# Kernel tuning notes

Measured on AMD Instinct MI355X. Metric: run time of the kernel, lower is better.

The kernel has to match this reference:

```python
import jax, jax.numpy as jnp
import numpy as np

SEQ, SUB, B, V = 32, 16, 512, 258
U = SEQ // SUB
Z, CH, CO, DH = 512, 1024, 512, 1024


def _lstm_cell(x, h, c, Wi, Wh, bi, bh):
    # torch gate order: input, forget, cell, output
    g = x @ Wi + h @ Wh + bi + bh  # [B, 4H]
    i, f, gg, o = jnp.split(g, 4, axis=-1)
    c = jax.nn.sigmoid(f) * c + jax.nn.sigmoid(i) * jnp.tanh(gg)
    h = jax.nn.sigmoid(o) * jnp.tanh(c)
    return h, c


def _lstm2(xs, h1_0, p1, p2):
    # xs: [T,B,in]; h1_0: [B,H] layer-1 initial hidden.
    # Layer-2 hidden and both cell states start at zero (initialize_state in torch code).
    z0 = jnp.zeros_like(h1_0)
    def step(carry, x):
        h1, c1, h2, c2 = carry
        h1, c1 = _lstm_cell(x, h1, c1, *p1)
        h2, c2 = _lstm_cell(h1, h2, c2, *p2)
        return (h1, c1, h2, c2), h2
    _, hs = jax.lax.scan(step, (h1_0, z0, z0, z0), xs)
    return hs  # [T,B,H] top-layer hidden states


def setup_inputs() -> dict:
    key = jax.random.key(0)
    ks = iter(jax.random.split(key, 40))
    def w(shape, s=0.05):
        return jax.random.normal(next(ks), shape, dtype=jnp.float32) * s
    return {
        "z": jax.random.normal(next(ks), (B, Z), dtype=jnp.float32),
        "x": jax.random.uniform(next(ks), (SEQ, B, V), dtype=jnp.float32),
        "conductor_input": w((1, B, V)),
        "ci_W": w((Z, CH)), "ci_b": w((CH,)),
        "cW1i": w((V, 4 * CH)), "cW1h": w((CH, 4 * CH)), "cb1i": w((4 * CH,)), "cb1h": w((4 * CH,)),
        "cW2i": w((CH, 4 * CH)), "cW2h": w((CH, 4 * CH)), "cb2i": w((4 * CH,)), "cb2h": w((4 * CH,)),
        "co_W": w((CH, CO)), "co_b": w((CO,)),
        "di_W": w((CO, DH)), "di_b": w((DH,)),
        "dW1i": w((CO + V, 4 * DH)), "dW1h": w((DH, 4 * DH)), "db1i": w((4 * DH,)), "db1h": w((4 * DH,)),
        "dW2i": w((DH, 4 * DH)), "dW2h": w((DH, 4 * DH)), "db2i": w((4 * DH,)), "db2h": w((4 * DH,)),
        "fc_W": w((DH, V)), "fc_b": w((V,)),
    }


def reference(z, x, conductor_input, ci_W, ci_b, cW1i, cW1h, cb1i, cb1h, cW2i, cW2h, cb2i, cb2h, co_W, co_b, di_W, di_b, dW1i, dW1h, db1i, db1h, dW2i, dW2h, db2i, db2h, fc_W, fc_b):
    # --- conductor: 2-layer LSTM over U steps of a learned constant input ---
    h1 = jnp.tanh(z @ ci_W + ci_b)  # [B,CH] layer-1 init hidden
    cin = jnp.broadcast_to(conductor_input, (U, B, V))
    ch = _lstm2(cin, h1, (cW1i, cW1h, cb1i, cb1h), (cW2i, cW2h, cb2i, cb2h))  # [U,B,CH]
    c = ch @ co_W + co_b  # [U,B,CO]
    # --- decoder (teacher forcing): state resets each sub-sequence, so the U
    # segments of length SUB are independent given c -> vmap over segments ---
    sos = jnp.zeros((1, B, V), jnp.float32).at[:, :, 0].set(1.0)
    prev = jnp.concatenate([sos, x[:-1]], axis=0).reshape(U, SUB, B, V)
    cb = jnp.broadcast_to(c[:, None], (U, SUB, B, CO))
    dec_in = jnp.concatenate([cb, prev], axis=-1)  # [U,SUB,B,CO+V]
    def run_seg(xs, cj):
        h1_0 = jnp.tanh(cj @ di_W + di_b)  # [B,DH]
        return _lstm2(xs, h1_0, (dW1i, dW1h, db1i, db1h), (dW2i, dW2h, db2i, db2h))
    hs = jax.vmap(run_seg)(dec_in, c)  # [U,SUB,B,DH]
    logp = jax.nn.log_softmax(hs @ fc_W + fc_b, axis=-1)  # log(softmax(.)) fused
    return logp.reshape(SEQ, B, V).transpose(1, 0, 2)  # [B,SEQ,V]
```

## Files before the change

### kernel.cpp

```cpp
#include <hip/hip_runtime.h>
#include <cstddef>
#include <cstdint>


namespace {

typedef short s8v __attribute__((ext_vector_type(8)));
typedef float f4v __attribute__((ext_vector_type(4)));
typedef unsigned short ushort_t;

__device__ inline unsigned short f2bf(float f) {
    union { float f; unsigned u; } v; v.f = f;
    unsigned r = v.u + 0x7fff + ((v.u >> 16) & 1);
    return (unsigned short)(r >> 16);
}
__device__ inline float bf2f(ushort_t u) {
    union { unsigned u; float f; } v; v.u = ((unsigned)u) << 16; return v.f;
}
__device__ inline float sigm_f(float x) { return 1.f / (1.f + __expf(-x)); }
__device__ inline float tanh_f(float x) {
    const float e = __expf(2.f * fabsf(x));
    return copysignf(1.f - 2.f / (e + 1.f), x);
}

#define GLOAD_LDS(gp, lp)                                              \
    __builtin_amdgcn_global_load_lds(                                  \
        (const __attribute__((address_space(1))) void*)(gp),           \
        (__attribute__((address_space(3))) void*)(lp), 16, 0, 0)

__device__ __forceinline__ void gemm_core(
    const ushort_t* __restrict__ A1a, const ushort_t* __restrict__ A1b,
    int lda1, int K1, const ushort_t* __restrict__ W1,
    const ushort_t* __restrict__ A2, int lda2, int K2,
    const ushort_t* __restrict__ W2,
    int bm, int bn, ushort_t* lds, f4v acc[4][4])
{
    const int tid = threadIdx.x;
    const int wid = tid >> 6;
    const int lane = tid & 63;
    const int wr = wid >> 1, wc = wid & 1;
    const int lrow = lane & 15, lkg = lane >> 4;

    const int n1 = K1 >> 5;
    const int n2 = (W2 != nullptr) ? (K2 >> 5) : 0;
    const int nt = n1 + n2;

    const int row0 = wid * 16 + (lane >> 2);
    const int row1 = row0 + 64;
    const int src0 = (((lane & 3) ^ ((row0 >> 1) & 3)) << 3);
    const int src1 = (((lane & 3) ^ ((row1 >> 1) & 3)) << 3);

    auto arow = [&](const ushort_t* Aa, const ushort_t* Ab, int lda,
                    int r) -> const ushort_t* {
        return (Ab != nullptr && r >= 512) ? Ab + (size_t)(r - 512) * lda
                                           : Aa + (size_t)r * lda;
    };
    const ushort_t* pA1q0 = arow(A1a, A1b, lda1, bm + row0) + src0;
    const ushort_t* pA1q1 = arow(A1a, A1b, lda1, bm + row1) + src1;
    const ushort_t* pA2q0 = nullptr;
    const ushort_t* pA2q1 = nullptr;
    if (n2 > 0) {
        pA2q0 = A2 + (size_t)(bm + row0) * lda2 + src0;
        pA2q1 = A2 + (size_t)(bm + row1) * lda2 + src1;
    }

    int sbuf = 2;
    auto stageA = [&](int idx, int buf) {
        const ushort_t *p0, *p1;
        if (idx < n1) { p0 = pA1q0 + (idx << 5); p1 = pA1q1 + (idx << 5); }
        else { const int i2 = idx - n1; p0 = pA2q0 + (i2 << 5); p1 = pA2q1 + (i2 << 5); }
        GLOAD_LDS(p0, lds + buf * 4096 + wid * 512);
        GLOAD_LDS(p1, lds + buf * 4096 + 2048 + wid * 512);
    };

    const int nb0 = (bn >> 4) + wc * 4;
    const ushort_t* W1l = W1 + (size_t)nb0 * n1 * 512 + lane * 8;
    const ushort_t* W2l = (n2 > 0) ? (W2 + (size_t)nb0 * n2 * 512 + lane * 8) : nullptr;

    auto loadB = [&](int t, s8v (&b)[4]) {
        const ushort_t* base; int kb, KB;
        if (t < n1) { base = W1l; kb = t; KB = n1; }
        else        { base = W2l; kb = t - n1; KB = n2; }
#pragma unroll
        for (int n = 0; n < 4; ++n)
            b[n] = *(const s8v*)(base + ((size_t)(n * KB + kb) << 9));
    };

    int aoff[4];
#pragma unroll
    for (int m = 0; m < 4; ++m) {
        const int r = wr * 64 + m * 16 + lrow;
        aoff[m] = r * 32 + ((lkg ^ ((r >> 1) & 3)) << 3);
    }

    s8v bA[4], bB[4];
    loadB(0, bA);
    stageA(0, 0);
    if (nt > 1) stageA(1, 1);

    int cbuf = 0;
    auto iter = [&](int t, s8v (&bcur)[4], s8v (&bnxt)[4]) {
        if (t + 1 < nt) loadB(t + 1, bnxt);
        if (t + 1 < nt) asm volatile("s_waitcnt vmcnt(6)" ::: "memory");
        else            asm volatile("s_waitcnt vmcnt(0)" ::: "memory");
        __builtin_amdgcn_s_barrier();
        __builtin_amdgcn_sched_barrier(0);
        if (t + 2 < nt) {
            stageA(t + 2, sbuf);
            sbuf = (sbuf == 2) ? 0 : sbuf + 1;
        }
        const ushort_t* L = lds + cbuf * 4096;
        s8v a[4];
#pragma unroll
        for (int m = 0; m < 4; ++m) a[m] = *(const s8v*)(L + aoff[m]);
        __builtin_amdgcn_s_setprio(1);
#pragma unroll
        for (int m = 0; m < 4; ++m)
#pragma unroll
            for (int n = 0; n < 4; ++n)
                acc[m][n] = __builtin_amdgcn_mfma_f32_16x16x32_bf16(
                    a[m], bcur[n], acc[m][n], 0, 0, 0);
        __builtin_amdgcn_s_setprio(0);
        cbuf = (cbuf == 2) ? 0 : cbuf + 1;
    };

    int t = 0;
    while (true) {
        iter(t, bA, bB); if (++t == nt) break;
        iter(t, bB, bA); if (++t == nt) break;
    }
}

template <int ACT>
__global__ __launch_bounds__(256, 2) void plain_gemm(
    const ushort_t* __restrict__ A, int lda, int K,
    const ushort_t* __restrict__ W,
    const float* __restrict__ bias, int bias_n,
    float* __restrict__ C, ushort_t* __restrict__ Cbf, int N)
{
    __shared__ __align__(16) ushort_t lds[3 * 4096];
    const int bm = blockIdx.x * 128, bn = blockIdx.y * 128;
    f4v acc[4][4] = {};
    gemm_core(A, nullptr, lda, K, W, nullptr, 0, 0, nullptr, bm, bn, lds, acc);

    const int tid = threadIdx.x, wid = tid >> 6, lane = tid & 63;
    const int wr = wid >> 1, wc = wid & 1, lrow = lane & 15, lkg = lane >> 4;
#pragma unroll
    for (int m = 0; m < 4; ++m) {
        const int row0 = bm + wr * 64 + m * 16 + lkg * 4;
#pragma unroll
        for (int n = 0; n < 4; ++n) {
            const int col = bn + wc * 64 + n * 16 + lrow;
            const float bv = (bias != nullptr && col < bias_n) ? bias[col] : 0.f;
#pragma unroll
            for (int r = 0; r < 4; ++r) {
                float v = acc[m][n][r] + bv;
                if (ACT == 1) v = tanh_f(v);
                const size_t o = (size_t)(row0 + r) * N + col;
                if (C != nullptr) C[o] = v;
                if (Cbf != nullptr) Cbf[o] = f2bf(v);
            }
        }
    }
}

struct Prob {
    const ushort_t* A1a; const ushort_t* A1b; int lda1; int K1;
    const ushort_t* B1t;
    const ushort_t* A2; int lda2; int K2; const ushort_t* B2t;
    const ushort_t* Dbf;
    const float* bias;
    float* cst;
    ushort_t* hout;
    ushort_t* hs;
    int step_s;
};

__global__ __launch_bounds__(256, 2) void lstm_step(Prob PA, int nxa, Prob PB,
                                                    int mshift)
{
    __shared__ __align__(16) ushort_t lds[3 * 4096];
    const int nblk = gridDim.x;
    const int wg = blockIdx.x;
    const int swz = (wg & 7) * (nblk >> 3) + (wg >> 3);
    const int nmb = 1 << mshift;
    const int nb = swz >> mshift;
    const int mb = swz & (nmb - 1);

    const bool isA = mb < nxa;
    const Prob& P = isA ? PA : PB;
    const int bm = (isA ? mb : mb - nxa) * 128;
    const int bn = nb * 128;

    f4v acc[4][4] = {};
    gemm_core(P.A1a, P.A1b, P.lda1, P.K1, P.B1t,
              P.A2, P.lda2, P.K2, P.B2t, bm, bn, lds, acc);

    const int tid = threadIdx.x, wid = tid >> 6, lane = tid & 63;
    const int wr = wid >> 1, wc = wid & 1, lrow = lane & 15, lkg = lane >> 4;
    const int colbase = bn + wc * 64;
    const int jb = (colbase >> 6) * 16 + lrow;

#pragma unroll
    for (int m = 0; m < 4; ++m) {
        const int row0 = bm + wr * 64 + m * 16 + lkg * 4;
#pragma unroll
        for (int r = 0; r < 4; ++r) {
            const int row = row0 + r;
            float g0 = acc[m][0][r], g1 = acc[m][1][r];
            float g2 = acc[m][2][r], g3 = acc[m][3][r];
            if (P.Dbf != nullptr) {
                const ushort_t* d = P.Dbf + (size_t)row * 4096 + colbase + lrow;
                g0 += bf2f(d[0]); g1 += bf2f(d[16]);
                g2 += bf2f(d[32]); g3 += bf2f(d[48]);
            }
            if (P.bias != nullptr) {
                const float* b = P.bias + colbase + lrow;
                g0 += b[0]; g1 += b[16]; g2 += b[32]; g3 += b[48];
            }
            const size_t ci = (size_t)row * 1024 + jb;
            const float cn = fmaf(sigm_f(g1), P.cst[ci], sigm_f(g0) * tanh_f(g2));
            const float hn = sigm_f(g3) * tanh_f(cn);
            P.cst[ci] = cn;
            const ushort_t hb = f2bf(hn);
            P.hout[ci] = hb;
            if (P.hs != nullptr) {
                size_t d;
                if (P.step_s >= 0) {
                    const int u = row >> 9, b = row & 511;
                    d = ((size_t)((u * 16 + P.step_s) * 512 + b) << 10) + jb;
                } else {
                    d = ci;
                }
                P.hs[d] = hb;
            }
        }
    }
}

template <int PERM>
__global__ __launch_bounds__(256) void pack_frag_bf16(
    const float* __restrict__ in, ushort_t* __restrict__ out,
    int K, int N, int Kp, int Np)
{
    __shared__ float tile[32][33];
    const int kb = blockIdx.x;
    const int np0 = blockIdx.y * 32;
    const int k0 = kb * 32;
    const int tx = threadIdx.x & 31;
    const int ty = threadIdx.x >> 5;
#pragma unroll
    for (int q = 0; q < 4; ++q) {
        const int k = k0 + ty + 8 * q;
        const int np = np0 + tx;
        int n;
        if (PERM) n = ((np >> 4) & 3) * 1024 + (np >> 6) * 16 + (np & 15);
        else      n = np;
        tile[ty + 8 * q][tx] = (k < K && n < N) ? in[(size_t)k * N + n] : 0.f;
    }
    __syncthreads();
    const int t = threadIdx.x;
    const int rec = t >> 7;
    const int lane = (t >> 1) & 63;
    const int half = t & 1;
    const size_t grec = (size_t)(np0 / 16 + rec) * (Kp / 32) + kb;
    const int kl = (lane >> 4) * 8 + half * 4;
    const int nl = rec * 16 + (lane & 15);
    ushort4 v;
    v.x = f2bf(tile[kl + 0][nl]);
    v.y = f2bf(tile[kl + 1][nl]);
    v.z = f2bf(tile[kl + 2][nl]);
    v.w = f2bf(tile[kl + 3][nl]);
    *(ushort4*)(out + (grec * 64 + lane) * 8 + half * 4) = v;
}

__global__ void convert_pad_bf16(const float* __restrict__ in,
                                 ushort_t* __restrict__ out,
                                 int K, int Kp, int total)
{
    const int idx = blockIdx.x * 256 + threadIdx.x;
    if (idx >= total) return;
    const int r = idx / Kp, k = idx - r * Kp;
    out[idx] = (k < K) ? f2bf(in[(size_t)r * K + k]) : (ushort_t)0;
}

__global__ void sos_init_bf16(ushort_t* __restrict__ sos)
{
    const int i = blockIdx.x * 256 + threadIdx.x;
    if (i < 512 * 320) sos[i] = ((i % 320) == 0) ? (ushort_t)0x3F80 : (ushort_t)0;
}

__global__ void permute_bias(const float* __restrict__ b1,
                             const float* __restrict__ b2,
                             float* __restrict__ out)
{
    const int c = blockIdx.x * 256 + threadIdx.x;
    if (c >= 4096) return;
    const int g = (c >> 4) & 3;
    const int j = (c >> 6) * 16 + (c & 15);
    out[c] = b1[g * 1024 + j] + b2[g * 1024 + j];
}

__global__ __launch_bounds__(256) void logsoftmax_kernel(
    const float* __restrict__ logits, float* __restrict__ out)
{
    const int row = blockIdx.x;
    const int tid = threadIdx.x;
    const float* L = logits + (size_t)row * 384;
    const int t = row >> 9;
    const int b = row & 511;
    float* O = out + ((size_t)b * 32 + t) * 258;

    const float x0 = L[tid];
    const float x1 = (tid < 2) ? L[256 + tid] : -1e30f;

    __shared__ float sm[4];
    float m = fmaxf(x0, x1);
#pragma unroll
    for (int off = 32; off > 0; off >>= 1) m = fmaxf(m, __shfl_down(m, off));
    if ((tid & 63) == 0) sm[tid >> 6] = m;
    __syncthreads();
    m = fmaxf(fmaxf(sm[0], sm[1]), fmaxf(sm[2], sm[3]));
    __syncthreads();

    float s = expf(x0 - m) + ((tid < 2) ? expf(x1 - m) : 0.f);
#pragma unroll
    for (int off = 32; off > 0; off >>= 1) s += __shfl_down(s, off);
    if ((tid & 63) == 0) sm[tid >> 6] = s;
    __syncthreads();
    s = sm[0] + sm[1] + sm[2] + sm[3];

    const float lse = m + logf(s);
    O[tid] = x0 - lse;
    if (tid < 2) O[256 + tid] = x1 - lse;
}

}

extern "C" void kernel_launch(void* const* d_in, const int* in_sizes, int n_in,
                              void* d_out, int out_size, void* d_ws, size_t ws_size,
                              hipStream_t stream)
{
    (void)in_sizes; (void)n_in; (void)out_size; (void)ws_size;

    const float* z    = (const float*)d_in[0];
    const float* x    = (const float*)d_in[1];
    const float* cin  = (const float*)d_in[2];
    const float* ciW  = (const float*)d_in[3];
    const float* cib  = (const float*)d_in[4];
    const float* cW1i = (const float*)d_in[5];
    const float* cW1h = (const float*)d_in[6];
    const float* cb1i = (const float*)d_in[7];
    const float* cb1h = (const float*)d_in[8];
    const float* cW2i = (const float*)d_in[9];
    const float* cW2h = (const float*)d_in[10];
    const float* cb2i = (const float*)d_in[11];
    const float* cb2h = (const float*)d_in[12];
    const float* coW  = (const float*)d_in[13];
    const float* cob  = (const float*)d_in[14];
    const float* diW  = (const float*)d_in[15];
    const float* dib  = (const float*)d_in[16];
    const float* dW1i = (const float*)d_in[17];
    const float* dW1h = (const float*)d_in[18];
    const float* db1i = (const float*)d_in[19];
    const float* db1h = (const float*)d_in[20];
    const float* dW2i = (const float*)d_in[21];
    const float* dW2h = (const float*)d_in[22];
    const float* db2i = (const float*)d_in[23];
    const float* db2h = (const float*)d_in[24];
    const float* fcW  = (const float*)d_in[25];
    const float* fcb  = (const float*)d_in[26];
    float* out = (float*)d_out;

    char* wsp = (char*)d_ws;
    size_t off = 0;
    auto allocf = [&](size_t n) { float* p = (float*)(wsp + off); off += n * 4; return p; };
    auto allocb = [&](size_t n) { ushort_t* p = (ushort_t*)(wsp + off); off += n * 2; return p; };

    float* cst = allocf((size_t)3 * 1024 * 1024 + 64);
    float* c1c = cst;
    float* c2c = cst + (size_t)512 * 1024;
    float* c1d = cst + (size_t)1024 * 1024;
    float* c2d = cst + (size_t)2 * 1024 * 1024;
    float* pb1c = allocf(4096);
    float* pb2c = allocf(4096);
    float* pb1d = allocf(4096);
    float* pb2d = allocf(4096);
    float* logits = allocf((size_t)16384 * 384);

    ushort_t* h2z  = allocb((size_t)2 * (512 + 1024) * 1024);
    ushort_t* hc2A = h2z;
    ushort_t* hc2B = h2z + (size_t)512 * 1024;
    ushort_t* h2dA = h2z + (size_t)2 * 512 * 1024;
    ushort_t* h2dB = h2z + (size_t)(2 * 512 + 1024) * 1024;

    ushort_t* hc1A = allocb((size_t)512 * 1024);
    ushort_t* hc1B = allocb((size_t)512 * 1024);
    ushort_t* h1dA = allocb((size_t)1024 * 1024);
    ushort_t* h1dB = allocb((size_t)1024 * 1024);

    ushort_t* zbf    = allocb((size_t)512 * 512);
    ushort_t* cinbf  = allocb((size_t)512 * 320);
    ushort_t* sosbf  = allocb((size_t)512 * 320);
    ushort_t* xbf    = allocb((size_t)16384 * 320);
    ushort_t* chbf   = allocb((size_t)1024 * 1024);
    ushort_t* ccode  = allocb((size_t)1024 * 512);
    ushort_t* cpre   = allocb((size_t)1024 * 4096);
    ushort_t* xW1c   = allocb((size_t)512 * 4096);
    ushort_t* hsbf   = allocb((size_t)16384 * 1024);

    ushort_t* ciWp  = allocb((size_t)1024 * 512);
    ushort_t* cW1ip = allocb((size_t)4096 * 320);
    ushort_t* cW1hp = allocb((size_t)4096 * 1024);
    ushort_t* cW2ip = allocb((size_t)4096 * 1024);
    ushort_t* cW2hp = allocb((size_t)4096 * 1024);
    ushort_t* coWp  = allocb((size_t)512 * 1024);
    ushort_t* dtopp = allocb((size_t)4096 * 512);
    ushort_t* dbotp = allocb((size_t)4096 * 320);
    ushort_t* diWp  = allocb((size_t)1024 * 512);
    ushort_t* dW1hp = allocb((size_t)4096 * 1024);
    ushort_t* dW2ip = allocb((size_t)4096 * 1024);
    ushort_t* dW2hp = allocb((size_t)4096 * 1024);
    ushort_t* fcWp  = allocb((size_t)384 * 1024);

    hipMemsetAsync(cst, 0, (size_t)3 * 1024 * 1024 * 4, stream);
    hipMemsetAsync(h2z, 0, (size_t)2 * (512 + 1024) * 1024 * 2, stream);

    auto pack = [&](const float* in, ushort_t* o, int K, int N, int Kp, int Np, int perm) {
        dim3 g(Kp / 32, Np / 32);
        if (perm) pack_frag_bf16<1><<<g, 256, 0, stream>>>(in, o, K, N, Kp, Np);
        else      pack_frag_bf16<0><<<g, 256, 0, stream>>>(in, o, K, N, Kp, Np);
    };
    pack(ciW, ciWp, 512, 1024, 512, 1024, 0);
    pack(cW1i, cW1ip, 258, 4096, 320, 4096, 1);
    pack(cW1h, cW1hp, 1024, 4096, 1024, 4096, 1);
    pack(cW2i, cW2ip, 1024, 4096, 1024, 4096, 1);
    pack(cW2h, cW2hp, 1024, 4096, 1024, 4096, 1);
    pack(coW, coWp, 1024, 512, 1024, 512, 0);
    pack(dW1i, dtopp, 512, 4096, 512, 4096, 1);
    pack(dW1i + (size_t)512 * 4096, dbotp, 258, 4096, 320, 4096, 1);
    pack(diW, diWp, 512, 1024, 512, 1024, 0);
    pack(dW1h, dW1hp, 1024, 4096, 1024, 4096, 1);
    pack(dW2i, dW2ip, 1024, 4096, 1024, 4096, 1);
    pack(dW2h, dW2hp, 1024, 4096, 1024, 4096, 1);
    pack(fcW, fcWp, 1024, 258, 1024, 384, 0);

    auto convert = [&](const float* in, ushort_t* o, int K, int Kp, int R) {
        const int total = R * Kp;
        convert_pad_bf16<<<dim3((total + 255) / 256), 256, 0, stream>>>(in, o, K, Kp, total);
    };
    convert(z, zbf, 512, 512, 512);
    convert(cin, cinbf, 258, 320, 512);
    convert(x, xbf, 258, 320, 16384);
    sos_init_bf16<<<dim3((512 * 320 + 255) / 256), 256, 0, stream>>>(sosbf);
    permute_bias<<<16, 256, 0, stream>>>(cb1i, cb1h, pb1c);
    permute_bias<<<16, 256, 0, stream>>>(cb2i, cb2h, pb2c);
    permute_bias<<<16, 256, 0, stream>>>(db1i, db1h, pb1d);
    permute_bias<<<16, 256, 0, stream>>>(db2i, db2h, pb2d);

    auto gemm = [&](int act, const ushort_t* A, int lda, int K, const ushort_t* W,
                    const float* bias, int bias_n,
                    float* C, ushort_t* Cbf, int M, int N) {
        dim3 g(M / 128, N / 128);
        if (act) plain_gemm<1><<<g, 256, 0, stream>>>(A, lda, K, W, bias, bias_n, C, Cbf, N);
        else     plain_gemm<0><<<g, 256, 0, stream>>>(A, lda, K, W, bias, bias_n, C, Cbf, N);
    };

    gemm(1, zbf, 512, 512, ciWp, cib, 1024, nullptr, hc1A, 512, 1024);
    gemm(0, cinbf, 320, 320, cW1ip, pb1c, 4096, nullptr, xW1c, 512, 4096);

    ushort_t* HC1[2] = {hc1A, hc1B};
    ushort_t* HC2[2] = {hc2A, hc2B};
    for (int k = 0; k <= 2; ++k) {
        Prob pa{}, pb{};
        int nxa = 0, nxb = 0;
        if (k < 2) {
            pa = {HC1[k & 1], nullptr, 1024, 1024, cW1hp,
                  nullptr, 0, 0, nullptr,
                  xW1c, nullptr, c1c, HC1[(k + 1) & 1], nullptr, -1};
            nxa = 4;
        }
        if (k >= 1) {
            pb = {HC1[k & 1], nullptr, 1024, 1024, cW2ip,
                  HC2[k & 1], 1024, 1024, cW2hp,
                  nullptr, pb2c, c2c, HC2[(k + 1) & 1],
                  chbf + (size_t)(k - 1) * 512 * 1024, -1};
            nxb = 4;
        }
        const int nmb = nxa + nxb;
        const int mshift = (nmb == 4) ? 2 : 3;
        lstm_step<<<dim3(nmb * 32), 256, 0, stream>>>(pa, nxa, pb, mshift);
    }

    gemm(0, chbf, 1024, 1024, coWp, cob, 512, nullptr, ccode, 1024, 512);
    gemm(0, ccode, 512, 512, dtopp, pb1d, 4096, nullptr, cpre, 1024, 4096);
    gemm(1, ccode, 512, 512, diWp, dib, 1024, nullptr, h1dA, 1024, 1024);

    ushort_t* H1[2] = {h1dA, h1dB};
    ushort_t* H2[2] = {h2dA, h2dB};
    for (int k = 0; k <= 16; ++k) {
        Prob pa{}, pb{};
        int nxa = 0, nxb = 0;
        if (k < 16) {
            const ushort_t* plo = (k == 0) ? sosbf : (xbf + (size_t)(k - 1) * 512 * 320);
            const ushort_t* phi = xbf + (size_t)(15 + k) * 512 * 320;
            pa = {plo, phi, 320, 320, dbotp,
                  H1[k & 1], 1024, 1024, dW1hp,
                  cpre, nullptr, c1d, H1[(k + 1) & 1], nullptr, -1};
            nxa = 8;
        }
        if (k >= 1) {
            pb = {H1[k & 1], nullptr, 1024, 1024, dW2ip,
                  H2[k & 1], 1024, 1024, dW2hp,
                  nullptr, pb2d, c2d, H2[(k + 1) & 1], hsbf, k - 1};
            nxb = 8;
        }
        const int nmb = nxa + nxb;
        const int mshift = (nmb == 8) ? 3 : 4;
        lstm_step<<<dim3(nmb * 32), 256, 0, stream>>>(pa, nxa, pb, mshift);
    }

    gemm(0, hsbf, 1024, 1024, fcWp, fcb, 258, logits, nullptr, 16384, 384);
    logsoftmax_kernel<<<dim3(16384), 256, 0, stream>>>(logits, out);
}
```

Measured before the change: 1.193 ms.

## Halve GEMM M-tile to 64 rows and deepen B-fragment prefetch to three stages

Shrinks the block tile from 128x128 to 64x128 in both the plain GEMM and the fused LSTM step kernel, doubling the number of workgroups per launch and raising launch bounds to allow 4 blocks per CU. The aim is better occupancy and more parallelism for the small per-step recurrent GEMMs, which previously launched too few blocks to fill the GPU. The B-operand register prefetch is also extended from double to triple buffering, issued two iterations ahead, with adjusted waitcnt thresholds. The trade-off is that each weight tile is loaded by twice as many blocks, lowering B reuse and increasing global/L2 traffic.

```diff
diff --git a/kernel.cpp b/kernel.cpp
--- a/kernel.cpp
+++ b/kernel.cpp
@@ -33,7 +33,7 @@
     int lda1, int K1, const ushort_t* __restrict__ W1,
     const ushort_t* __restrict__ A2, int lda2, int K2,
     const ushort_t* __restrict__ W2,
-    int bm, int bn, ushort_t* lds, f4v acc[4][4])
+    int bm, int bn, ushort_t* lds, f4v acc[2][4])
 {
     const int tid = threadIdx.x;
     const int wid = tid >> 6;
@@ -45,32 +45,23 @@
     const int n2 = (W2 != nullptr) ? (K2 >> 5) : 0;
     const int nt = n1 + n2;
 
-    const int row0 = wid * 16 + (lane >> 2);
-    const int row1 = row0 + 64;
-    const int src0 = (((lane & 3) ^ ((row0 >> 1) & 3)) << 3);
-    const int src1 = (((lane & 3) ^ ((row1 >> 1) & 3)) << 3);
+    const int srow = wid * 16 + (lane >> 2);
+    const int ssrc = (((lane & 3) ^ ((srow >> 1) & 3)) << 3);
 
     auto arow = [&](const ushort_t* Aa, const ushort_t* Ab, int lda,
                     int r) -> const ushort_t* {
         return (Ab != nullptr && r >= 512) ? Ab + (size_t)(r - 512) * lda
                                            : Aa + (size_t)r * lda;
     };
-    const ushort_t* pA1q0 = arow(A1a, A1b, lda1, bm + row0) + src0;
-    const ushort_t* pA1q1 = arow(A1a, A1b, lda1, bm + row1) + src1;
-    const ushort_t* pA2q0 = nullptr;
-    const ushort_t* pA2q1 = nullptr;
-    if (n2 > 0) {
-        pA2q0 = A2 + (size_t)(bm + row0) * lda2 + src0;
-        pA2q1 = A2 + (size_t)(bm + row1) * lda2 + src1;
-    }
-
-    int sbuf = 2;
+    const ushort_t* pA1 = arow(A1a, A1b, lda1, bm + srow) + ssrc;
+    const ushort_t* pA2 = nullptr;
+    if (n2 > 0) pA2 = A2 + (size_t)(bm + srow) * lda2 + ssrc;
+
     auto stageA = [&](int idx, int buf) {
-        const ushort_t *p0, *p1;
-        if (idx < n1) { p0 = pA1q0 + (idx << 5); p1 = pA1q1 + (idx << 5); }
-        else { const int i2 = idx - n1; p0 = pA2q0 + (i2 << 5); p1 = pA2q1 + (i2 << 5); }
-        GLOAD_LDS(p0, lds + buf * 4096 + wid * 512);
-        GLOAD_LDS(p1, lds + buf * 4096 + 2048 + wid * 512);
+        const ushort_t* p;
+        if (idx < n1) p = pA1 + (idx << 5);
+        else          p = pA2 + ((idx - n1) << 5);
+        GLOAD_LDS(p, lds + buf * 2048 + wid * 512);
     };
 
     const int nb0 = (bn >> 4) + wc * 4;
@@ -86,36 +77,37 @@
             b[n] = *(const s8v*)(base + ((size_t)(n * KB + kb) << 9));
     };
 
-    int aoff[4];
-#pragma unroll
-    for (int m = 0; m < 4; ++m) {
-        const int r = wr * 64 + m * 16 + lrow;
+    int aoff[2];
+#pragma unroll
+    for (int m = 0; m < 2; ++m) {
+        const int r = wr * 32 + m * 16 + lrow;
         aoff[m] = r * 32 + ((lkg ^ ((r >> 1) & 3)) << 3);
     }
 
-    s8v bA[4], bB[4];
-    loadB(0, bA);
+    s8v b0[4], b1[4], b2[4];
+    loadB(0, b0);
     stageA(0, 0);
-    if (nt > 1) stageA(1, 1);
-
-    int cbuf = 0;
-    auto iter = [&](int t, s8v (&bcur)[4], s8v (&bnxt)[4]) {
-        if (t + 1 < nt) loadB(t + 1, bnxt);
-        if (t + 1 < nt) asm volatile("s_waitcnt vmcnt(6)" ::: "memory");
+    loadB(1, b1);
+    stageA(1, 1);
+
+    int cbuf = 0, sbuf = 2;
+    auto iter = [&](int t, s8v (&bcur)[4], s8v (&bpre)[4]) {
+        if (t + 1 < nt) asm volatile("s_waitcnt vmcnt(5)" ::: "memory");
         else            asm volatile("s_waitcnt vmcnt(0)" ::: "memory");
         __builtin_amdgcn_s_barrier();
         __builtin_amdgcn_sched_barrier(0);
         if (t + 2 < nt) {
             stageA(t + 2, sbuf);
+            loadB(t + 2, bpre);
             sbuf = (sbuf == 2) ? 0 : sbuf + 1;
         }
-        const ushort_t* L = lds + cbuf * 4096;
-        s8v a[4];
-#pragma unroll
-        for (int m = 0; m < 4; ++m) a[m] = *(const s8v*)(L + aoff[m]);
+        const ushort_t* L = lds + cbuf * 2048;
+        s8v a[2];
+#pragma unroll
+        for (int m = 0; m < 2; ++m) a[m] = *(const s8v*)(L + aoff[m]);
         __builtin_amdgcn_s_setprio(1);
 #pragma unroll
-        for (int m = 0; m < 4; ++m)
+        for (int m = 0; m < 2; ++m)
 #pragma unroll
             for (int n = 0; n < 4; ++n)
                 acc[m][n] = __builtin_amdgcn_mfma_f32_16x16x32_bf16(
@@ -126,28 +118,29 @@
 
     int t = 0;
     while (true) {
-        iter(t, bA, bB); if (++t == nt) break;
-        iter(t, bB, bA); if (++t == nt) break;
+        iter(t, b0, b2); if (++t == nt) break;
+        iter(t, b1, b0); if (++t == nt) break;
+        iter(t, b2, b1); if (++t == nt) break;
     }
 }
 
 template <int ACT>
-__global__ __launch_bounds__(256, 2) void plain_gemm(
+__global__ __launch_bounds__(256, 4) void plain_gemm(
     const ushort_t* __restrict__ A, int lda, int K,
     const ushort_t* __restrict__ W,
     const float* __restrict__ bias, int bias_n,
     float* __restrict__ C, ushort_t* __restrict__ Cbf, int N)
 {
-    __shared__ __align__(16) ushort_t lds[3 * 4096];
-    const int bm = blockIdx.x * 128, bn = blockIdx.y * 128;
-    f4v acc[4][4] = {};
+    __shared__ __align__(16) ushort_t lds[3 * 2048];
+    const int bm = blockIdx.x * 64, bn = blockIdx.y * 128;
+    f4v acc[2][4] = {};
     gemm_core(A, nullptr, lda, K, W, nullptr, 0, 0, nullptr, bm, bn, lds, acc);
 
     const int tid = threadIdx.x, wid = tid >> 6, lane = tid & 63;
     const int wr = wid >> 1, wc = wid & 1, lrow = lane & 15, lkg = lane >> 4;
 #pragma unroll
-    for (int m = 0; m < 4; ++m) {
-        const int row0 = bm + wr * 64 + m * 16 + lkg * 4;
+    for (int m = 0; m < 2; ++m) {
+        const int row0 = bm + wr * 32 + m * 16 + lkg * 4;
 #pragma unroll
         for (int n = 0; n < 4; ++n) {
             const int col = bn + wc * 64 + n * 16 + lrow;
@@ -176,10 +169,10 @@
     int step_s;
 };
 
-__global__ __launch_bounds__(256, 2) void lstm_step(Prob PA, int nxa, Prob PB,
+__global__ __launch_bounds__(256, 4) void lstm_step(Prob PA, int nxa, Prob PB,
                                                     int mshift)
 {
-    __shared__ __align__(16) ushort_t lds[3 * 4096];
+    __shared__ __align__(16) ushort_t lds[3 * 2048];
     const int nblk = gridDim.x;
     const int wg = blockIdx.x;
     const int swz = (wg & 7) * (nblk >> 3) + (wg >> 3);
@@ -189,10 +182,10 @@
 
     const bool isA = mb < nxa;
     const Prob& P = isA ? PA : PB;
-    const int bm = (isA ? mb : mb - nxa) * 128;
+    const int bm = (isA ? mb : mb - nxa) * 64;
     const int bn = nb * 128;
 
-    f4v acc[4][4] = {};
+    f4v acc[2][4] = {};
     gemm_core(P.A1a, P.A1b, P.lda1, P.K1, P.B1t,
               P.A2, P.lda2, P.K2, P.B2t, bm, bn, lds, acc);
 
@@ -202,8 +195,8 @@
     const int jb = (colbase >> 6) * 16 + lrow;
 
 #pragma unroll
-    for (int m = 0; m < 4; ++m) {
-        const int row0 = bm + wr * 64 + m * 16 + lkg * 4;
+    for (int m = 0; m < 2; ++m) {
+        const int row0 = bm + wr * 32 + m * 16 + lkg * 4;
 #pragma unroll
         for (int r = 0; r < 4; ++r) {
             const int row = row0 + r;
@@ -461,7 +454,7 @@
     auto gemm = [&](int act, const ushort_t* A, int lda, int K, const ushort_t* W,
                     const float* bias, int bias_n,
                     float* C, ushort_t* Cbf, int M, int N) {
-        dim3 g(M / 128, N / 128);
+        dim3 g(M / 64, N / 128);
         if (act) plain_gemm<1><<<g, 256, 0, stream>>>(A, lda, K, W, bias, bias_n, C, Cbf, N);
         else     plain_gemm<0><<<g, 256, 0, stream>>>(A, lda, K, W, bias, bias_n, C, Cbf, N);
     };
@@ -478,17 +471,17 @@
             pa = {HC1[k & 1], nullptr, 1024, 1024, cW1hp,
                   nullptr, 0, 0, nullptr,
                   xW1c, nullptr, c1c, HC1[(k + 1) & 1], nullptr, -1};
-            nxa = 4;
+            nxa = 8;
         }
         if (k >= 1) {
             pb = {HC1[k & 1], nullptr, 1024, 1024, cW2ip,
                   HC2[k & 1], 1024, 1024, cW2hp,
                   nullptr, pb2c, c2c, HC2[(k + 1) & 1],
                   chbf + (size_t)(k - 1) * 512 * 1024, -1};
-            nxb = 4;
+            nxb = 8;
         }
         const int nmb = nxa + nxb;
-        const int mshift = (nmb == 4) ? 2 : 3;
+        const int mshift = (nmb == 8) ? 3 : 4;
         lstm_step<<<dim3(nmb * 32), 256, 0, stream>>>(pa, nxa, pb, mshift);
     }
 
@@ -507,16 +500,16 @@
             pa = {plo, phi, 320, 320, dbotp,
                   H1[k & 1], 1024, 1024, dW1hp,
                   cpre, nullptr, c1d, H1[(k + 1) & 1], nullptr, -1};
-            nxa = 8;
+            nxa = 16;
         }
         if (k >= 1) {
             pb = {H1[k & 1], nullptr, 1024, 1024, dW2ip,
                   H2[k & 1], 1024, 1024, dW2hp,
                   nullptr, pb2d, c2d, H2[(k + 1) & 1], hsbf, k - 1};
-            nxb = 8;
+            nxb = 16;
         }
         const int nmb = nxa + nxb;
-        const int mshift = (nmb == 8) ? 3 : 4;
+        const int mshift = (nmb == 16) ? 4 : 5;
         lstm_step<<<dim3(nmb * 32), 256, 0, stream>>>(pa, nxa, pb, mshift);
     }
 
```

Measured after the change: 4.485 ms. 276% more time.
